# Performance work log

Hardware: AMD Instinct MI355X
Metric: run time of the kernel (lower is better)

Reference implementation:

```python
import jax, jax.numpy as jnp
from jax import lax
import numpy as np

WAY = 100
SHOT = 5
QUERY = 15
D = 4096
LAM = 10.0
ALPHA = 0.2
N_EPOCHS = 20
EPS = 1e-6
MAXITERS = 1000
N_L = WAY * SHOT          # 500 labeled
N_U = WAY * QUERY         # 1500 unlabeled
N_TOT = N_L + N_U         # 2000


def setup_inputs() -> dict:
    key = jax.random.key(0)
    kx, = jax.random.split(key, 1)
    X = jax.random.uniform(kx, (N_TOT, D), dtype=jnp.float32)  # features must be >= 0
    # data is ordered as (shot+query) blocks of `way` samples, one per class
    labels = jnp.tile(jnp.arange(WAY, dtype=jnp.int32), SHOT + QUERY)
    return {"X": X, "labels": labels}


def _normalize(X):
    # F.normalize(p=2, dim=-1) with eps=1e-12
    return X / jnp.maximum(jnp.linalg.norm(X, axis=-1, keepdims=True), 1e-12)


def _cdist(X, Y):
    # Euclidean distances [n, m] via gram trick (avoids [n, m, d] intermediate)
    d2 = (X * X).sum(-1)[:, None] + (Y * Y).sum(-1)[None, :] - 2.0 * (X @ Y.T)
    return jnp.sqrt(jnp.maximum(d2, 1e-12))


def _sinkhorn(M, r, c):
    # Row/col scaling loop of compute_optimal_transport, tracked via scaling
    # vectors (a, b) so P_k = a * K * b exactly matches the in-place updates.
    K = jnp.exp(-LAM * M)
    K = K / K.sum()
    n, m = M.shape

    def step(carry, _):
        a, b, prev, done = carry
        rowsum = a * (K @ b)                       # P.sum(-1)
        err = jnp.max(jnp.abs(prev - rowsum))      # convergence check vs old u
        done = done | (err <= EPS)
        a_new = jnp.where(done, a, a * r / rowsum)
        colsum = b * (K.T @ a_new)                 # P.sum(1) after row scaling
        b_new = jnp.where(done, b, b * c / colsum)
        prev_new = jnp.where(done, prev, rowsum)
        return (a_new, b_new, prev_new, done), None

    init = (jnp.ones(n, M.dtype), jnp.ones(m, M.dtype),
            jnp.zeros(n, M.dtype), jnp.array(False))
    (a, b, _, _), _ = lax.scan(step, init, None, length=MAXITERS)
    return a[:, None] * K * b[None, :]


def _forward(X, labels):
    # power transform
    X = jnp.sqrt(X + 1e-6)
    # scale (mode='val'): normalize -> center labeled/unlabeled separately -> normalize
    X = _normalize(X)
    Xl = X[:N_L] - X[:N_L].mean(0, keepdims=True)
    Xu = X[N_L:] - X[N_L:].mean(0, keepdims=True)
    Z = _normalize(jnp.concatenate([Xl, Xu], axis=0))

    # init class means from labeled shots
    mus0 = Z.reshape(SHOT + QUERY, WAY, -1)[:SHOT].mean(0)  # [way, d]

    r = jnp.ones(N_U, Z.dtype)
    c = jnp.full((WAY,), float(QUERY), Z.dtype)
    onehot = jax.nn.one_hot(labels[:N_L], WAY, dtype=Z.dtype)

    def get_probas(mus):
        dist = _cdist(Z, mus)                      # [n_tot, way]
        Pu = _sinkhorn(dist[N_L:], r, c)           # [n_u, way]
        return jnp.concatenate([onehot, Pu], axis=0)

    def epoch(mus, _):
        p = get_probas(mus)
        emus = (p.T @ Z) / p.sum(0)[:, None]       # estimate_from_mask
        return mus + ALPHA * (emus - mus), None    # update_from_estimate

    mus, _ = lax.scan(epoch, mus0, None, length=N_EPOCHS)

    P = get_probas(mus)
    logP = jnp.log(P[N_L:] + 1e-5)
    acc = (jnp.argmax(P[N_L:], axis=-1) == labels[N_L:]).astype(jnp.float32).mean()
    return logP, acc


def reference(X, labels):
    return _forward(X, labels)
```

## Files before the change

kernel.cpp:

```cpp
#include <hip/hip_runtime.h>

#define WAY   100
#define SHOT  5
#define NQ    15
#define DD    4096
#define N_L   500
#define N_U   1500
#define N_TOT 2000
#define LAMF  10.0f
#define EPSF  1e-6f
#define MAXIT 1000

#define OFF_Z      0u
#define OFF_CPP    3145728u
#define OFF_MEANL  8192000u
#define OFF_MEANU  8196096u
#define OFF_SL     8200192u
#define OFF_MUSA   8609792u
#define OFF_MUSB   9068544u
#define OFF_MUSQP  9527296u
#define OFF_MUSB16 9552896u
#define OFF_PTH    9782272u
#define OFF_PTL    9868288u
#define OFF_KMAT   9954304u
#define OFF_COLS   10104320u
#define OFF_MISC   10113920u
#define OFF_ZUT    10114688u
#define OFF_ZUTL   13260416u
#define OFF_AG     16406144u
#define OFF_PREVG  16407680u
#define OFF_BINIT  16409216u

#define SINK_BLOCKS 16
#define SINK_T 512
#define RPB 94
#define CPR 12
#define PTS 1536
#define CPS 409600u

typedef __attribute__((ext_vector_type(8))) short short8_t;
typedef __attribute__((ext_vector_type(4))) float f32x4;

__device__ __forceinline__ short f2bs(float f) {
  unsigned u = __float_as_uint(f);
  unsigned r = (u + 0x7FFFu + ((u >> 16) & 1u)) >> 16;
  return (short)r;
}
__device__ __forceinline__ float bs2f(short s) {
  return __uint_as_float(((unsigned)(unsigned short)s) << 16);
}

__device__ __forceinline__ float ld_agent(const float* p) {
  return __hip_atomic_load(p, __ATOMIC_RELAXED, __HIP_MEMORY_SCOPE_AGENT);
}
__device__ __forceinline__ void st_agent(float* p, float v) {
  __hip_atomic_store(p, v, __ATOMIC_RELAXED, __HIP_MEMORY_SCOPE_AGENT);
}

__global__ __launch_bounds__(256) void k_pow_norm(const float* __restrict__ X, float* __restrict__ Z,
                                                  float* __restrict__ msums, unsigned* __restrict__ misc_u,
                                                  float* __restrict__ aG) {
  int i = blockIdx.x, tid = threadIdx.x;
  __shared__ float red[256];
  if (i < 32) msums[i * 256 + tid] = 0.f;
  if (i == 32) { misc_u[tid] = 0u; misc_u[tid + 256] = 0u; misc_u[tid + 512] = 0u; }
  if (i == 33) { for (int z = tid; z < 1504; z += 256) aG[z] = -1.f; }
  const float* x = X + (size_t)i * DD;
  float s = 0.f;
  for (int k = tid; k < DD; k += 256) s += x[k] + 1e-6f;
  red[tid] = s; __syncthreads();
  for (int o = 128; o > 0; o >>= 1) { if (tid < o) red[tid] += red[tid + o]; __syncthreads(); }
  float inv = 1.0f / fmaxf(sqrtf(red[0]), 1e-12f);
  float* z = Z + (size_t)i * DD;
  for (int k = tid; k < DD; k += 256) z[k] = sqrtf(x[k] + 1e-6f) * inv;
}

__global__ __launch_bounds__(256) void k_colmeans(const float* __restrict__ Z, float* __restrict__ mLs,
                                                  float* __restrict__ mUs) {
  int k = blockIdx.x * 256 + threadIdx.x;
  int r0 = blockIdx.y * 80;
  float sL = 0.f, sU = 0.f;
  for (int r = r0; r < r0 + 80; ++r) {
    float v = Z[(size_t)r * DD + k];
    if (r < N_L) sL += v; else sU += v;
  }
  if (r0 < N_L) atomicAdd(&mLs[k], sL);
  if (r0 + 80 > N_L) atomicAdd(&mUs[k], sU);
}

__global__ __launch_bounds__(256) void k_center(float* __restrict__ Z, const float* __restrict__ mLs,
                                                const float* __restrict__ mUs) {
  int i = blockIdx.x, tid = threadIdx.x;
  __shared__ float red[256];
  const float* m = (i < N_L) ? mLs : mUs;
  const float scale = (i < N_L) ? (1.0f / 500.0f) : (1.0f / 1500.0f);
  float* z = Z + (size_t)i * DD;
  float s = 0.f;
  for (int k = tid; k < DD; k += 256) { float v = z[k] - m[k] * scale; s += v * v; }
  red[tid] = s; __syncthreads();
  for (int o = 128; o > 0; o >>= 1) { if (tid < o) red[tid] += red[tid + o]; __syncthreads(); }
  float inv = 1.0f / fmaxf(sqrtf(red[0]), 1e-12f);
  for (int k = tid; k < DD; k += 256) z[k] = (z[k] - m[k] * scale) * inv;
}

__global__ __launch_bounds__(256) void k_musinit(const float* __restrict__ Z, float* __restrict__ SL,
                                                 float* __restrict__ mus, short* __restrict__ musb,
                                                 float* __restrict__ musqP, float* __restrict__ binit,
                                                 short* __restrict__ PTH, short* __restrict__ PTL) {
  int w = blockIdx.x, tid = threadIdx.x;
  __shared__ float red[256];
  if (tid == 0) binit[w] = 1.0f;
  if (tid >= 4 && tid < 8) PTH[(size_t)w * PTS + 1500 + (tid - 4)] = 0;
  if (tid >= 8 && tid < 12) PTL[(size_t)w * PTS + 1500 + (tid - 8)] = 0;
  float q = 0.f;
  for (int k = tid; k < DD; k += 256) {
    float s = 0.f;
    for (int sh = 0; sh < SHOT; ++sh) s += Z[(size_t)(sh * WAY + w) * DD + k];
    SL[(size_t)w * DD + k] = s;
    float m = s / 5.0f;
    mus[(size_t)w * DD + k] = m;
    musb[(size_t)w * DD + k] = f2bs(m);
    q += m * m;
  }
  red[tid] = q; __syncthreads();
  for (int o = 128; o > 0; o >>= 1) { if (tid < o) red[tid] += red[tid + o]; __syncthreads(); }
  if (tid == 0) musqP[(size_t)w * 256] = red[0];
  else musqP[(size_t)w * 256 + tid] = 0.f;
}

__global__ __launch_bounds__(256) void k_zb(const float* __restrict__ Z, short* __restrict__ Zb, int ubase) {
  size_t i0 = (size_t)ubase * DD + ((size_t)blockIdx.x * 256 + threadIdx.x) * 8;
  short8_t v;
  if (i0 < (size_t)N_U * DD) {
    const float* src = Z + (size_t)N_L * DD + i0;
    float4 a = *(const float4*)src;
    float4 b = *(const float4*)(src + 4);
    v[0] = f2bs(a.x); v[1] = f2bs(a.y); v[2] = f2bs(a.z); v[3] = f2bs(a.w);
    v[4] = f2bs(b.x); v[5] = f2bs(b.y); v[6] = f2bs(b.z); v[7] = f2bs(b.w);
  } else {
    v = (short8_t){0, 0, 0, 0, 0, 0, 0, 0};
  }
  *(short8_t*)(Zb + i0) = v;
}

__global__ __launch_bounds__(256) void k_zt(const float* __restrict__ Z, short* __restrict__ ZTH,
                                            short* __restrict__ ZTL) {
  __shared__ float tile[32][33];
  int k0 = blockIdx.x * 32, u0 = blockIdx.y * 32;
  int c = threadIdx.x & 31, r0 = threadIdx.x >> 5;
#pragma unroll
  for (int rr = 0; rr < 4; ++rr) {
    int r = r0 + rr * 8;
    int u = u0 + r;
    tile[r][c] = (u < N_U) ? Z[(size_t)(N_L + u) * DD + k0 + c] : 0.f;
  }
  __syncthreads();
#pragma unroll
  for (int rr = 0; rr < 4; ++rr) {
    int r = r0 + rr * 8;
    float v = tile[c][r];
    short hi = f2bs(v);
    ZTH[(size_t)(k0 + r) * PTS + u0 + c] = hi;
    ZTL[(size_t)(k0 + r) * PTS + u0 + c] = f2bs(v - bs2f(hi));
  }
}

__global__ __launch_bounds__(256) void k_gemm1K(const short* __restrict__ Zb, const short* __restrict__ musb,
                                                const float* __restrict__ musqP, float* __restrict__ Kmat,
                                                unsigned* __restrict__ misc_u) {
  int tid = threadIdx.x;
  __shared__ float redA[4 * 7 * 4 * 64];
  __shared__ float musq2[2][128];
  if (blockIdx.x == 0) {
    for (int z = tid; z < 768; z += 256) misc_u[z] = 0u;
  }
  {
    int w = tid >> 1, half = tid & 1;
    if (w < WAY) {
      const float* mp = musqP + (size_t)w * 256 + half * 128;
      float q = 0.f;
#pragma unroll 4
      for (int bb = 0; bb < 128; bb += 4) {
        float4 v4 = *(const float4*)(mp + bb);
        q += (v4.x + v4.y) + (v4.z + v4.w);
      }
      musq2[half][w] = q;
    }
  }
  int wv = tid >> 6, l = tid & 63;
  int l15 = l & 15, quad = (l >> 4) & 3;
  int u0 = blockIdx.x * 16;
  f32x4 acc[7];
#pragma unroll
  for (int c = 0; c < 7; ++c) acc[c] = (f32x4){0.f, 0.f, 0.f, 0.f};

  const short* bp = Zb + (size_t)(u0 + l15) * DD + wv * 1024 + quad * 8;
  const short* ap = musb + (size_t)l15 * DD + wv * 1024 + quad * 8;
#pragma unroll 2
  for (int kc = 0; kc < 1024; kc += 32) {
    short8_t bf = *(const short8_t*)(bp + kc);
#pragma unroll
    for (int c = 0; c < 7; ++c) {
      short8_t af = *(const short8_t*)(ap + (size_t)c * 16 * DD + kc);
      acc[c] = __builtin_amdgcn_mfma_f32_16x16x32_bf16(af, bf, acc[c], 0, 0, 0);
    }
  }
#pragma unroll
  for (int c = 0; c < 7; ++c)
#pragma unroll
    for (int r = 0; r < 4; ++r)
      redA[((wv * 7 + c) * 4 + r) * 64 + l] = acc[c][r];
  __syncthreads();
  if (wv == 0) {
    int u = u0 + l15;
#pragma unroll
    for (int c = 0; c < 7; ++c)
#pragma unroll
      for (int r = 0; r < 4; ++r) {
        int base = (c * 4 + r) * 64 + l;
        float s = redA[base] + redA[base + 1792] + redA[base + 3584] + redA[base + 5376];
        int w = 16 * c + quad * 4 + r;
        if (w < WAY && u < N_U) {
          float d2 = 1.0f + (musq2[0][w] + musq2[1][w]) - 2.0f * s;
          Kmat[(size_t)u * WAY + w] = expf(-LAMF * sqrtf(fmaxf(d2, 1e-12f)));
        }
      }
  }
}

__device__ __forceinline__ void gbar(unsigned* slots, unsigned t) {
  __syncthreads();
  if (threadIdx.x == 0) {
    asm volatile("s_waitcnt vmcnt(0) lgkmcnt(0)" ::: "memory");
    __hip_atomic_store(slots + (unsigned)blockIdx.x * 16, t, __ATOMIC_RELAXED, __HIP_MEMORY_SCOPE_AGENT);
  }
  if (threadIdx.x < SINK_BLOCKS) {
    while (__hip_atomic_load(slots + threadIdx.x * 16, __ATOMIC_ACQUIRE, __HIP_MEMORY_SCOPE_AGENT) < t)
      __builtin_amdgcn_s_sleep(1);
  }
  __syncthreads();
}

__global__ __launch_bounds__(SINK_T) void k_sink(const float* __restrict__ Kg,
                                                 short* __restrict__ PTH, short* __restrict__ PTL,
                                                 float* __restrict__ colsP, float* __restrict__ aG,
                                                 float* __restrict__ prevG, float* __restrict__ binit,
                                                 unsigned* __restrict__ misc_u, float* __restrict__ misc_f,
                                                 const int* __restrict__ labels, float* __restrict__ out,
                                                 int finalmode) {
  __shared__ float Kl[RPB * 100];
  __shared__ float4 bS4[25];
  __shared__ float a[RPB], aold[RPB], prevs[RPB];
  __shared__ float rerr[SINK_T];
  __shared__ float c2[800];
  __shared__ float red[SINK_T];
  __shared__ float eSh;
  float* bS = (float*)bS4;
  unsigned* slots = misc_u + 8;
  float* KsumG = misc_f + 3;
  int tid = threadIdx.x;
  int row0 = (int)blockIdx.x * RPB;
  int nrows = (blockIdx.x == SINK_BLOCKS - 1) ? (N_U - row0) : RPB;

  bool warm = (aG[row0] >= 0.f);

  float ks = 0.f;
  int n4 = nrows * 25;
  const float4* Ksrc = (const float4*)(Kg + (size_t)row0 * 100);
  for (int i = tid; i < n4; i += SINK_T) {
    float4 v = Ksrc[i];
    *(float4*)(&Kl[i * 4]) = v;
    ks += (v.x + v.y) + (v.z + v.w);
  }
  if (!warm) {
    red[tid] = ks; __syncthreads();
    for (int o = SINK_T / 2; o > 0; o >>= 1) { if (tid < o) red[tid] += red[tid + o]; __syncthreads(); }
    if (tid == 0) atomicAdd(KsumG, red[0]);
  }
  if (tid < WAY) bS[tid] = binit[tid];

  unsigned bt = 0;
  if (!warm) { ++bt; gbar(slots, bt); }
  float S = warm ? 1.f : ld_agent(KsumG);
  if (tid < nrows) {
    a[tid] = warm ? aG[row0 + tid] : (1.0f / S);
    prevs[tid] = warm ? prevG[row0 + tid] : 0.f;
  }

  bool conv = false;
  for (int t = 0; t < MAXIT; ++t) {
    float* cp = colsP + (t & 1) * 2048;
    __syncthreads();
    if (tid < nrows) {
      const float* kr = &Kl[tid * 100];
      float4 ac = {0.f, 0.f, 0.f, 0.f};
#pragma unroll
      for (int j4 = 0; j4 < 25; ++j4) {
        float4 bv = bS4[j4];
        float4 kv = *(const float4*)(kr + j4 * 4);
        ac.x = fmaf(kv.x, bv.x, ac.x); ac.y = fmaf(kv.y, bv.y, ac.y);
        ac.z = fmaf(kv.z, bv.z, ac.z); ac.w = fmaf(kv.w, bv.w, ac.w);
      }
      float rs = ((ac.x + ac.y) + (ac.z + ac.w)) * a[tid];
      rerr[tid] = fabsf(prevs[tid] - rs);
      aold[tid] = a[tid];
      a[tid] = a[tid] / rs;
      prevs[tid] = rs;
    } else {
      rerr[tid] = 0.f;
    }
    __syncthreads();
    if (tid < 200) {
      int j4 = tid % 25, ch = tid / 25;
      int rlo = ch * CPR, rhi = rlo + CPR; if (rhi > nrows) rhi = nrows;
      float4 pa = {0.f, 0.f, 0.f, 0.f};
      for (int r = rlo; r < rhi; ++r) {
        float4 kv = *(const float4*)(&Kl[r * 100 + j4 * 4]);
        float av = a[r];
        pa.x = fmaf(kv.x, av, pa.x); pa.y = fmaf(kv.y, av, pa.y);
        pa.z = fmaf(kv.z, av, pa.z); pa.w = fmaf(kv.w, av, pa.w);
      }
      *(float4*)(&c2[ch * 100 + j4 * 4]) = pa;
    }
    if (tid >= 448) {
      int t6 = tid & 63;
      float m = rerr[t6];
#pragma unroll
      for (int k = 1; k < 8; ++k) m = fmaxf(m, rerr[t6 + 64 * k]);
#pragma unroll
      for (int o = 32; o > 0; o >>= 1) m = fmaxf(m, __shfl_down(m, o));
      if (t6 == 0) st_agent(cp + (unsigned)blockIdx.x * 128 + 100, m);
    }
    __syncthreads();
    if (tid < WAY) {
      float s = ((c2[tid] + c2[100 + tid]) + (c2[200 + tid] + c2[300 + tid])) +
                ((c2[400 + tid] + c2[500 + tid]) + (c2[600 + tid] + c2[700 + tid]));
      st_agent(cp + (unsigned)blockIdx.x * 128 + tid, s);
    }
    ++bt;
    gbar(slots, bt);
    float bnew = 0.f;
    if (tid >= 256 && tid < 256 + WAY) {
      int j = tid - 256;
      float s = 0.f;
#pragma unroll
      for (int sb = 0; sb < SINK_BLOCKS; ++sb) s += ld_agent(cp + sb * 128 + j);
      bnew = (float)NQ / s;
    }
    if (tid < 64) {
      float e = (tid < SINK_BLOCKS) ? ld_agent(cp + tid * 128 + 100) : 0.f;
#pragma unroll
      for (int o = 8; o > 0; o >>= 1) e = fmaxf(e, __shfl_down(e, o));
      if (tid == 0) eSh = e;
    }
    __syncthreads();
    if (eSh <= EPSF) { conv = true; break; }
    if (tid >= 256 && tid < 256 + WAY) bS[tid - 256] = bnew;
  }
  __syncthreads();

  if (finalmode) {
    for (int idx = tid; idx < nrows * WAY; idx += SINK_T) {
      int r = idx / WAY, j = idx - r * WAY;
      float av = conv ? aold[r] : a[r];
      float p = av * Kl[r * 100 + j] * bS[j];
      out[(size_t)(row0 + r) * WAY + j] = logf(p + 1e-5f);
    }
    if (tid < nrows) {
      const float* kr = &Kl[tid * 100];
      int am = 0; float bv = kr[0] * bS[0];
      for (int j = 1; j < WAY; ++j) { float p = kr[j] * bS[j]; if (p > bv) { bv = p; am = j; } }
      if (am == labels[N_L + row0 + tid]) atomicAdd(misc_u + 5, 1u);
    }
    return;
  }

  if (tid < nrows) {
    float af = conv ? aold[tid] : a[tid];
    aG[row0 + tid] = af;
    prevG[row0 + tid] = prevs[tid];
  }
  if (blockIdx.x == 0 && tid < WAY) binit[tid] = bS[tid];
  for (int idx = tid; idx < WAY * nrows; idx += SINK_T) {
    int j = idx / nrows; int r = idx - j * nrows;
    float av = conv ? aold[r] : a[r];
    float p = av * Kl[r * 100 + j] * bS[j];
    short hi = f2bs(p);
    PTH[(size_t)j * PTS + row0 + r] = hi;
    PTL[(size_t)j * PTS + row0 + r] = f2bs(p - bs2f(hi));
  }
}

__global__ __launch_bounds__(64) void k_gemm2(const short* __restrict__ PTH, const short* __restrict__ PTL,
                                              const short* __restrict__ ZTH, const short* __restrict__ ZTL,
                                              float* __restrict__ CPp) {
  int l = threadIdx.x, l15 = l & 15, quad = l >> 4;
  int k0 = blockIdx.x * 16;
  int us = blockIdx.y;
  int kcb = us * 192;
  int kce = (us == 7) ? 1504 : kcb + 192;
  f32x4 acc[7];
#pragma unroll
  for (int c = 0; c < 7; ++c) acc[c] = (f32x4){0.f, 0.f, 0.f, 0.f};
  size_t aoff = (size_t)l15 * PTS + quad * 8;
  const short* bph = ZTH + (size_t)(k0 + l15) * PTS + quad * 8;
  const short* bpl = ZTL + (size_t)(k0 + l15) * PTS + quad * 8;
  for (int kc = kcb; kc < kce; kc += 32) {
    short8_t bh = *(const short8_t*)(bph + kc);
    short8_t bl = *(const short8_t*)(bpl + kc);
#pragma unroll
    for (int c = 0; c < 7; ++c) {
      short8_t ah = *(const short8_t*)(PTH + aoff + (size_t)c * 16 * PTS + kc);
      short8_t al = *(const short8_t*)(PTL + aoff + (size_t)c * 16 * PTS + kc);
      acc[c] = __builtin_amdgcn_mfma_f32_16x16x32_bf16(ah, bh, acc[c], 0, 0, 0);
      acc[c] = __builtin_amdgcn_mfma_f32_16x16x32_bf16(al, bh, acc[c], 0, 0, 0);
      acc[c] = __builtin_amdgcn_mfma_f32_16x16x32_bf16(ah, bl, acc[c], 0, 0, 0);
    }
  }
  float* dst = CPp + (size_t)us * CPS;
#pragma unroll
  for (int c = 0; c < 7; ++c)
#pragma unroll
    for (int r = 0; r < 4; ++r) {
      int w = 16 * c + quad * 4 + r;
      if (w < WAY) dst[(size_t)w * DD + k0 + l15] = acc[c][r];
    }
}

__global__ __launch_bounds__(256) void k_musup(const float* __restrict__ musR, const float* __restrict__ SL,
                                               const float* __restrict__ CPp, float* __restrict__ musW,
                                               short* __restrict__ musb, float* __restrict__ musqP) {
  int w = blockIdx.x, tid = threadIdx.x;
  int kb = blockIdx.y * 1024;
  __shared__ float red[256];
  float q = 0.f;
  for (int k = kb + tid; k < kb + 1024; k += 256) {
    size_t o = (size_t)w * DD + k;
    float c = 0.f;
#pragma unroll
    for (int s = 0; s < 8; ++s) c += CPp[(size_t)s * CPS + o];
    float emus = (SL[o] + c) / 20.0f;
    float m = musR[o];
    float v = m + 0.2f * (emus - m);
    musW[o] = v;
    musb[o] = f2bs(v);
    q += v * v;
  }
  red[tid] = q; __syncthreads();
  for (int o = 128; o > 0; o >>= 1) { if (tid < o) red[tid] += red[tid + o]; __syncthreads(); }
  if (tid == 0) musqP[(size_t)w * 256 + blockIdx.y] = red[0];
}

__global__ void k_acc(const unsigned* __restrict__ ctr, float* __restrict__ out) {
  if (threadIdx.x == 0) out[N_U * WAY] = (float)(*ctr) / 1500.0f;
}

extern "C" void kernel_launch(void* const* d_in, const int* in_sizes, int n_in,
                              void* d_out, int out_size, void* d_ws, size_t ws_size,
                              hipStream_t stream) {
  const float* X = (const float*)d_in[0];
  const int* labels = (const int*)d_in[1];
  float* out = (float*)d_out;
  float* ws = (float*)d_ws;

  float* Z     = ws + OFF_Z;
  short* Zb    = (short*)(ws + OFF_Z);
  float* CPp   = ws + OFF_CPP;
  float* meanL = ws + OFF_MEANL;
  float* meanU = ws + OFF_MEANU;
  float* SL    = ws + OFF_SL;
  float* musA  = ws + OFF_MUSA;
  float* musB  = ws + OFF_MUSB;
  float* musqP = ws + OFF_MUSQP;
  short* musb16 = (short*)(ws + OFF_MUSB16);
  short* PTH   = (short*)(ws + OFF_PTH);
  short* PTL   = (short*)(ws + OFF_PTL);
  float* Kmat  = ws + OFF_KMAT;
  float* colsP = ws + OFF_COLS;
  float* misc_f = ws + OFF_MISC;
  unsigned* misc_u = (unsigned*)(ws + OFF_MISC);
  short* ZTH   = (short*)(ws + OFF_ZUT);
  short* ZTL   = (short*)(ws + OFF_ZUTL);
  float* aG    = ws + OFF_AG;
  float* prevG = ws + OFF_PREVG;
  float* binit = ws + OFF_BINIT;

  k_pow_norm<<<N_TOT, 256, 0, stream>>>(X, Z, meanL, misc_u, aG);
  k_colmeans<<<dim3(16, 25), 256, 0, stream>>>(Z, meanL, meanU);
  k_center<<<N_TOT, 256, 0, stream>>>(Z, meanL, meanU);
  k_musinit<<<WAY, 256, 0, stream>>>(Z, SL, musA, musb16, musqP, binit, PTH, PTL);
  k_zt<<<dim3(128, 48), 256, 0, stream>>>(Z, ZTH, ZTL);
  k_zb<<<1536, 256, 0, stream>>>(Z, Zb, 0);
  k_zb<<<1536, 256, 0, stream>>>(Z, Zb, 768);

  float* musR = musA;
  float* musW = musB;
  for (int e = 0; e < 20; ++e) {
    k_gemm1K<<<96, 256, 0, stream>>>(Zb, musb16, musqP, Kmat, misc_u);
    k_sink<<<SINK_BLOCKS, SINK_T, 0, stream>>>(Kmat, PTH, PTL, colsP, aG, prevG, binit, misc_u, misc_f,
                                               labels, out, 0);
    k_gemm2<<<dim3(256, 8), 64, 0, stream>>>(PTH, PTL, ZTH, ZTL, CPp);
    k_musup<<<dim3(WAY, 4), 256, 0, stream>>>(musR, SL, CPp, musW, musb16, musqP);
    float* tmp = musR; musR = musW; musW = tmp;
  }
  k_gemm1K<<<96, 256, 0, stream>>>(Zb, musb16, musqP, Kmat, misc_u);
  k_sink<<<SINK_BLOCKS, SINK_T, 0, stream>>>(Kmat, PTH, PTL, colsP, aG, prevG, binit, misc_u, misc_f,
                                             labels, out, 1);
  k_acc<<<1, 64, 0, stream>>>(misc_u + 5, out);
}
```

Before: 1.964 ms.

## Replace per-iteration grid barrier in Sinkhorn with per-block tagged flag polling

Inside the Sinkhorn loop, the global barrier is replaced by per-block iteration tags written next to each block's partial column sums. Each reader polls the tags, and column-sum accumulation proceeds block by block as tags arrive, with a shared-memory flag fan-out. The goal is to cut grid-barrier latency from every one of up to a thousand iterations. The cost is more polling traffic and extra tag resets in the earlier kernels. Correctness relies on acquire ordering and on the double-buffered slots being reset before each launch.

```diff
diff --git a/kernel.cpp b/kernel.cpp
--- a/kernel.cpp
+++ b/kernel.cpp
@@ -59,12 +59,14 @@
 
 __global__ __launch_bounds__(256) void k_pow_norm(const float* __restrict__ X, float* __restrict__ Z,
                                                   float* __restrict__ msums, unsigned* __restrict__ misc_u,
-                                                  float* __restrict__ aG) {
+                                                  float* __restrict__ aG, float* __restrict__ colsP) {
   int i = blockIdx.x, tid = threadIdx.x;
   __shared__ float red[256];
   if (i < 32) msums[i * 256 + tid] = 0.f;
   if (i == 32) { misc_u[tid] = 0u; misc_u[tid + 256] = 0u; misc_u[tid + 512] = 0u; }
   if (i == 33) { for (int z = tid; z < 1504; z += 256) aG[z] = -1.f; }
+  if (i == 34 && tid < 32)
+    st_agent(colsP + (tid >> 4) * 2048 + (tid & 15) * 128 + 101, 0.f);
   const float* x = X + (size_t)i * DD;
   float s = 0.f;
   for (int k = tid; k < DD; k += 256) s += x[k] + 1e-6f;
@@ -167,12 +169,14 @@
 
 __global__ __launch_bounds__(256) void k_gemm1K(const short* __restrict__ Zb, const short* __restrict__ musb,
                                                 const float* __restrict__ musqP, float* __restrict__ Kmat,
-                                                unsigned* __restrict__ misc_u) {
+                                                unsigned* __restrict__ misc_u, float* __restrict__ colsP) {
   int tid = threadIdx.x;
   __shared__ float redA[4 * 7 * 4 * 64];
   __shared__ float musq2[2][128];
   if (blockIdx.x == 0) {
     for (int z = tid; z < 768; z += 256) misc_u[z] = 0u;
+    if (tid < 32)
+      st_agent(colsP + (tid >> 4) * 2048 + (tid & 15) * 128 + 101, 0.f);
   }
   {
     int w = tid >> 1, half = tid & 1;
@@ -255,6 +259,7 @@
   __shared__ float c2[800];
   __shared__ float red[SINK_T];
   __shared__ float eSh;
+  __shared__ int tagf[SINK_BLOCKS];
   float* bS = (float*)bS4;
   unsigned* slots = misc_u + 8;
   float* KsumG = misc_f + 3;
@@ -263,6 +268,7 @@
   int nrows = (blockIdx.x == SINK_BLOCKS - 1) ? (N_U - row0) : RPB;
 
   bool warm = (aG[row0] >= 0.f);
+  if (tid < SINK_BLOCKS) tagf[tid] = 0;
 
   float ks = 0.f;
   int n4 = nrows * 25;
@@ -279,8 +285,7 @@
   }
   if (tid < WAY) bS[tid] = binit[tid];
 
-  unsigned bt = 0;
-  if (!warm) { ++bt; gbar(slots, bt); }
+  if (!warm) gbar(slots, 1u);
   float S = warm ? 1.f : ld_agent(KsumG);
   if (tid < nrows) {
     a[tid] = warm ? aG[row0 + tid] : (1.0f / S);
@@ -337,21 +342,35 @@
                 ((c2[400 + tid] + c2[500 + tid]) + (c2[600 + tid] + c2[700 + tid]));
       st_agent(cp + (unsigned)blockIdx.x * 128 + tid, s);
     }
-    ++bt;
-    gbar(slots, bt);
+    __syncthreads();
+    if (tid == 0)
+      __hip_atomic_store((unsigned*)(cp + (unsigned)blockIdx.x * 128 + 101), (unsigned)(t + 1),
+                         __ATOMIC_RELAXED, __HIP_MEMORY_SCOPE_AGENT);
+    float epoll = 0.f;
+    if (tid < SINK_BLOCKS) {
+      const unsigned* tp = (const unsigned*)(cp + tid * 128 + 101);
+      while (__hip_atomic_load(tp, __ATOMIC_ACQUIRE, __HIP_MEMORY_SCOPE_AGENT) < (unsigned)(t + 1))
+        __builtin_amdgcn_s_sleep(1);
+      __hip_atomic_store(&tagf[tid], t + 1, __ATOMIC_RELEASE, __HIP_MEMORY_SCOPE_WORKGROUP);
+      epoll = ld_agent(cp + tid * 128 + 100);
+    }
+    if (tid < 64) {
+      float e = epoll;
+#pragma unroll
+      for (int o = 8; o > 0; o >>= 1) e = fmaxf(e, __shfl_down(e, o));
+      if (tid == 0) eSh = e;
+    }
     float bnew = 0.f;
     if (tid >= 256 && tid < 256 + WAY) {
       int j = tid - 256;
       float s = 0.f;
 #pragma unroll
-      for (int sb = 0; sb < SINK_BLOCKS; ++sb) s += ld_agent(cp + sb * 128 + j);
+      for (int sb = 0; sb < SINK_BLOCKS; ++sb) {
+        while (__hip_atomic_load(&tagf[sb], __ATOMIC_ACQUIRE, __HIP_MEMORY_SCOPE_WORKGROUP) < t + 1)
+          __builtin_amdgcn_s_sleep(1);
+        s += ld_agent(cp + sb * 128 + j);
+      }
       bnew = (float)NQ / s;
-    }
-    if (tid < 64) {
-      float e = (tid < SINK_BLOCKS) ? ld_agent(cp + tid * 128 + 100) : 0.f;
-#pragma unroll
-      for (int o = 8; o > 0; o >>= 1) e = fmaxf(e, __shfl_down(e, o));
-      if (tid == 0) eSh = e;
     }
     __syncthreads();
     if (eSh <= EPSF) { conv = true; break; }
@@ -485,7 +504,7 @@
   float* prevG = ws + OFF_PREVG;
   float* binit = ws + OFF_BINIT;
 
-  k_pow_norm<<<N_TOT, 256, 0, stream>>>(X, Z, meanL, misc_u, aG);
+  k_pow_norm<<<N_TOT, 256, 0, stream>>>(X, Z, meanL, misc_u, aG, colsP);
   k_colmeans<<<dim3(16, 25), 256, 0, stream>>>(Z, meanL, meanU);
   k_center<<<N_TOT, 256, 0, stream>>>(Z, meanL, meanU);
   k_musinit<<<WAY, 256, 0, stream>>>(Z, SL, musA, musb16, musqP, binit, PTH, PTL);
@@ -496,14 +515,14 @@
   float* musR = musA;
   float* musW = musB;
   for (int e = 0; e < 20; ++e) {
-    k_gemm1K<<<96, 256, 0, stream>>>(Zb, musb16, musqP, Kmat, misc_u);
+    k_gemm1K<<<96, 256, 0, stream>>>(Zb, musb16, musqP, Kmat, misc_u, colsP);
     k_sink<<<SINK_BLOCKS, SINK_T, 0, stream>>>(Kmat, PTH, PTL, colsP, aG, prevG, binit, misc_u, misc_f,
                                                labels, out, 0);
     k_gemm2<<<dim3(256, 8), 64, 0, stream>>>(PTH, PTL, ZTH, ZTL, CPp);
     k_musup<<<dim3(WAY, 4), 256, 0, stream>>>(musR, SL, CPp, musW, musb16, musqP);
     float* tmp = musR; musR = musW; musW = tmp;
   }
-  k_gemm1K<<<96, 256, 0, stream>>>(Zb, musb16, musqP, Kmat, misc_u);
+  k_gemm1K<<<96, 256, 0, stream>>>(Zb, musb16, musqP, Kmat, misc_u, colsP);
   k_sink<<<SINK_BLOCKS, SINK_T, 0, stream>>>(Kmat, PTH, PTL, colsP, aG, prevG, binit, misc_u, misc_f,
                                              labels, out, 1);
   k_acc<<<1, 64, 0, stream>>>(misc_u + 5, out);
```

Result: no change. 1.972 ms (+0.4%).
